# Kernel optimization log

Measured on AMD Instinct MI355X. Metric: run time of the kernel, lower is better.

## Reference

```python
import jax, jax.numpy as jnp
import numpy as np

B, V, J, NS, NE = 2048, 5023, 5, 100, 50
PB = 9 * (J - 1)  # pose basis = 36


def setup_inputs() -> dict:
    key = jax.random.key(0)
    ks = jax.random.split(key, 8)
    jr = jax.random.uniform(ks[5], (J, V), dtype=jnp.float32)
    lw = jax.random.uniform(ks[6], (V, J), dtype=jnp.float32)
    return {
        "shape_params": jax.random.normal(ks[0], (B, NS), dtype=jnp.float32),
        "expression_params": jax.random.normal(ks[1], (B, NE), dtype=jnp.float32),
        "pose": jax.random.normal(ks[2], (B, J * 3), dtype=jnp.float32) * 0.2,
        "v_template": jax.random.normal(ks[3], (V, 3), dtype=jnp.float32) * 0.1,
        "shapedirs": jax.random.normal(ks[4], (V, 3, NS + NE), dtype=jnp.float32) * 0.01,
        "posedirs": jax.random.normal(ks[7], (PB, V * 3), dtype=jnp.float32) * 0.01,
        "J_regressor": jr / jnp.sum(jr, axis=1, keepdims=True),   # rows sum to 1 (convex combos)
        "lbs_weights": lw / jnp.sum(lw, axis=1, keepdims=True),   # rows sum to 1 (skinning weights)
        "parents": np.array([0, 0, 1, 1, 1], dtype=np.int64),     # FLAME kintree (root entry unused)
    }


def batch_rodrigues(rot_vecs):
    """(N,3) axis-angle -> (N,3,3) rotation matrices (matches torch ref incl. +1e-8)."""
    angle = jnp.linalg.norm(rot_vecs + 1e-8, axis=1, keepdims=True)      # (N,1)
    rd = rot_vecs / angle
    cos = jnp.cos(angle)[:, :, None]                                      # (N,1,1)
    sin = jnp.sin(angle)[:, :, None]
    rx, ry, rz = rd[:, 0], rd[:, 1], rd[:, 2]
    z = jnp.zeros_like(rx)
    K = jnp.stack([z, -rz, ry, rz, z, -rx, -ry, rx, z], axis=1).reshape(-1, 3, 3)
    I = jnp.eye(3, dtype=rot_vecs.dtype)
    return I + sin * K + (1.0 - cos) * jnp.matmul(K, K)


def reference(shape_params, expression_params, pose, v_template, shapedirs,
              posedirs, J_regressor, lbs_weights, parents):
    par = np.asarray(parents)  # static kinematic tree
    b = shape_params.shape[0]
    betas = jnp.concatenate([shape_params, expression_params], axis=1)     # (B,150)
    v_shaped = v_template + jnp.einsum('bl,vkl->bvk', betas, shapedirs)    # (B,V,3)
    Jts = jnp.einsum('bvk,jv->bjk', v_shaped, J_regressor)                 # (B,J,3)
    # pose -> rotations, pose-corrective offsets
    rot_mats = batch_rodrigues(pose.reshape(-1, 3)).reshape(b, -1, 3, 3)   # (B,J,3,3)
    I3 = jnp.eye(3, dtype=pose.dtype)
    pose_feature = (rot_mats[:, 1:] - I3).reshape(b, -1)                   # (B,36)
    pose_offsets = jnp.matmul(pose_feature, posedirs).reshape(b, -1, 3)    # (B,V,3)
    v_posed = v_posed = pose_offsets + v_shaped
    # kinematic chain (relative joint transforms -> world transforms)
    rel_joints = jnp.concatenate(
        [Jts[:, :1], Jts[:, 1:] - Jts[:, par[1:]]], axis=1)                # (B,J,3)
    top = jnp.concatenate([rot_mats, rel_joints[..., None]], axis=-1)      # (B,J,3,4)
    bottom = jnp.broadcast_to(
        jnp.array([0., 0., 0., 1.], dtype=pose.dtype), (b, Jts.shape[1], 1, 4))
    tm = jnp.concatenate([top, bottom], axis=2)                            # (B,J,4,4)
    chain = [tm[:, 0]]
    for i in range(1, par.shape[0]):  # tiny fixed loop over 5 joints
        chain.append(jnp.matmul(chain[int(par[i])], tm[:, i]))
    transforms = jnp.stack(chain, axis=1)                                  # (B,J,4,4)
    posed_joints = transforms[:, :, :3, 3]
    # remove rest-pose joint locations: subtract (transforms @ [j;0]) from last column
    tj = jnp.einsum('bjmn,bjn->bjm', transforms[:, :, :, :3], Jts)         # (B,J,4)
    rel_transforms = transforms.at[:, :, :, 3].add(-tj)                    # (B,J,4,4)
    # linear blend skinning
    T = jnp.einsum('vj,bjmn->bvmn', lbs_weights, rel_transforms)           # (B,V,4,4)
    verts = jnp.einsum('bvmn,bvn->bvm', T[:, :, :3, :3], v_posed) + T[:, :, :3, 3]
    return verts, posed_joints
```

## Files before the change

### kernel.cpp

```cpp
#include <hip/hip_runtime.h>
#include <hip/hip_bf16.h>
#include <math.h>

#define B_N 2048
#define V_N 5023
#define V3_N 15069
#define NSJB 157
#define CHUNK 32

typedef float f32x4 __attribute__((ext_vector_type(4)));
typedef short short8 __attribute__((ext_vector_type(8)));

static __device__ __forceinline__ ushort f2bf(float f) {
  __hip_bfloat16 h = __float2bfloat16(f);
  return *reinterpret_cast<ushort*>(&h);
}

__global__ __launch_bounds__(256) void k_pre(const float* __restrict__ sdirs,
                                             const float* __restrict__ pdirs,
                                             const float* __restrict__ vtemp,
                                             const float* __restrict__ Jr,
                                             const float* __restrict__ shp,
                                             const float* __restrict__ expr,
                                             ushort* __restrict__ basis,
                                             float* __restrict__ part,
                                             ushort* __restrict__ bb) {
  __shared__ float Sh[16][452];
  __shared__ float Pd[36][48];
  int t = threadIdx.x, blk = blockIdx.x;
  if (blk < 314) {
    int bx = blk, v0 = bx * 16;
    for (int idx = t; idx < 16 * 450; idx += 256) {
      int r = idx / 450, c = idx - r * 450;
      int v = v0 + r;
      Sh[r][c] = (v < V_N) ? sdirs[(size_t)v * 450 + c] : 0.0f;
    }
    for (int idx = t; idx < 36 * 48; idx += 256) {
      int p = idx / 48, c = idx - p * 48;
      int v3 = v0 * 3 + c;
      Pd[p][c] = (v3 < V3_N) ? pdirs[(size_t)p * V3_N + v3] : 0.0f;
    }
    __syncthreads();
    for (int idx = t; idx < 64 * 96; idx += 256) {
      int row = idx / 96, kp = idx - row * 96;
      int vl = row >> 2, c = row & 3;
      int k0 = kp * 2;
      float f0 = 0.0f, f1 = 0.0f;
      if (c < 3) {
        if (k0 < 150) {
          f0 = Sh[vl][c * 150 + k0];
          f1 = Sh[vl][c * 150 + k0 + 1];
        } else if (k0 < 186) {
          f0 = Pd[k0 - 150][vl * 3 + c];
          f1 = Pd[k0 - 149][vl * 3 + c];
        }
      }
      uint u = (uint)f2bf(f0) | ((uint)f2bf(f1) << 16);
      ((uint*)basis)[(size_t)(bx * 64 + row) * 96 + kp] = u;
    }
  } else if (blk < 314 + NSJB) {
    float (*JrL)[CHUNK] = (float(*)[CHUNK]) & Sh[0][0];
    int bk = blk - 314;
    int vstart = bk * CHUNK;
    int cnt = min(CHUNK, V_N - vstart);
    for (int idx = t; idx < 5 * CHUNK; idx += 256) {
      int j = idx / CHUNK, vi = idx % CHUNK;
      JrL[j][vi] = (vi < cnt) ? Jr[j * V_N + vstart + vi] : 0.0f;
    }
    __syncthreads();
    float acc0[5] = {0, 0, 0, 0, 0}, acc1[5] = {0, 0, 0, 0, 0};
    int c0 = t, c1 = t + 256;
#pragma unroll 4
    for (int vi = 0; vi < CHUNK; ++vi) {
      int v = min(vstart + vi, V_N - 1);
      float val0 = sdirs[(size_t)v * 450 + c0];
      float val1 = 0.0f;
      if (c1 < 450) val1 = sdirs[(size_t)v * 450 + c1];
      else if (c1 < 453) val1 = vtemp[(size_t)v * 3 + (c1 - 450)];
#pragma unroll
      for (int j = 0; j < 5; ++j) {
        float w = JrL[j][vi];
        acc0[j] = fmaf(w, val0, acc0[j]);
        acc1[j] = fmaf(w, val1, acc1[j]);
      }
    }
    float* prow = part + (size_t)bk * 2280;
#pragma unroll
    for (int j = 0; j < 5; ++j) {
      prow[j * 456 + c0] = acc0[j];
      if (c1 < 453) prow[j * 456 + c1] = acc1[j];
    }
  } else {
    int idx = (blk - 314 - NSJB) * 256 + t;
    int b = idx / 96, cp = idx - b * 96;
    int c0 = cp * 2;
    float f0 = 0.0f, f1 = 0.0f;
    if (c0 < 100) {
      f0 = shp[(size_t)b * 100 + c0];
      f1 = shp[(size_t)b * 100 + c0 + 1];
    } else if (c0 < 150) {
      f0 = expr[(size_t)b * 50 + (c0 - 100)];
      f1 = expr[(size_t)b * 50 + (c0 - 99)];
    }
    ((uint*)bb)[idx] = (uint)f2bf(f0) | ((uint)f2bf(f1) << 16);
  }
}

__global__ void k_sj_reduce(const float* __restrict__ part, float* __restrict__ SJ) {
  int id = blockIdx.x * 256 + threadIdx.x;
  if (id >= 2280) return;
  int c = id % 456;
  if (c >= 453) return;
  float s = 0.0f;
  for (int bk = 0; bk < NSJB; ++bk) s += part[(size_t)bk * 2280 + id];
  SJ[id] = s;
}

__global__ __launch_bounds__(256) void k_jpose(const float* __restrict__ shp,
                                               const float* __restrict__ expr,
                                               const float* __restrict__ SJ,
                                               const float* __restrict__ pose,
                                               ushort* __restrict__ bb,
                                               float* __restrict__ A,
                                               float* __restrict__ out) {
  __shared__ float JtL[16][16];
  int t = threadIdx.x;
  int g = t >> 4, r = t & 15;
  int b = blockIdx.x * 16 + g;
  if (r < 15) {
    int j = r / 3, k = r - j * 3;
    const float* SJr = SJ + j * 456;
    float acc = SJr[450 + k];
    const float* srow = shp + (size_t)b * 100;
    const float* erow = expr + (size_t)b * 50;
    for (int l = 0; l < 100; ++l) acc = fmaf(srow[l], SJr[k * 150 + l], acc);
    for (int l = 0; l < 50; ++l) acc = fmaf(erow[l], SJr[k * 150 + 100 + l], acc);
    JtL[g][r] = acc;
  }
  __syncthreads();
  if (r != 0) return;
  float R[5][3][3];
#pragma unroll
  for (int j = 0; j < 5; ++j) {
    float rx = pose[(size_t)b * 15 + j * 3 + 0];
    float ry = pose[(size_t)b * 15 + j * 3 + 1];
    float rz = pose[(size_t)b * 15 + j * 3 + 2];
    float sx = rx + 1e-8f, sy = ry + 1e-8f, sz = rz + 1e-8f;
    float ang = sqrtf(sx * sx + sy * sy + sz * sz);
    float inv = 1.0f / ang;
    float ux = rx * inv, uy = ry * inv, uz = rz * inv;
    float c = cosf(ang), s = sinf(ang), omc = 1.0f - c;
    float K[3][3] = {{0.0f, -uz, uy}, {uz, 0.0f, -ux}, {-uy, ux, 0.0f}};
#pragma unroll
    for (int m = 0; m < 3; ++m)
#pragma unroll
      for (int n = 0; n < 3; ++n) {
        float k2 = 0.0f;
#pragma unroll
        for (int q = 0; q < 3; ++q) k2 += K[m][q] * K[q][n];
        R[j][m][n] = ((m == n) ? 1.0f : 0.0f) + s * K[m][n] + omc * k2;
      }
  }
  {
    float pf[36];
#pragma unroll
    for (int j = 1; j < 5; ++j)
#pragma unroll
      for (int m = 0; m < 3; ++m)
#pragma unroll
        for (int n = 0; n < 3; ++n)
          pf[(j - 1) * 9 + m * 3 + n] = R[j][m][n] - ((m == n) ? 1.0f : 0.0f);
    uint* bbu = (uint*)bb + (size_t)b * 96 + 75;
#pragma unroll
    for (int q = 0; q < 18; ++q)
      bbu[q] = (uint)f2bf(pf[2 * q]) | ((uint)f2bf(pf[2 * q + 1]) << 16);
  }
  float Jt[5][3];
#pragma unroll
  for (int j = 0; j < 5; ++j)
#pragma unroll
    for (int k = 0; k < 3; ++k) Jt[j][k] = JtL[g][j * 3 + k];
  const int par[5] = {0, 0, 1, 1, 1};
  float rel[5][3];
#pragma unroll
  for (int k = 0; k < 3; ++k) rel[0][k] = Jt[0][k];
#pragma unroll
  for (int j = 1; j < 5; ++j)
#pragma unroll
    for (int k = 0; k < 3; ++k) rel[j][k] = Jt[j][k] - Jt[par[j]][k];
  float Rg[5][3][3], tg[5][3];
#pragma unroll
  for (int m = 0; m < 3; ++m) {
#pragma unroll
    for (int n = 0; n < 3; ++n) Rg[0][m][n] = R[0][m][n];
    tg[0][m] = rel[0][m];
  }
#pragma unroll
  for (int j = 1; j < 5; ++j) {
    int p = par[j];
#pragma unroll
    for (int m = 0; m < 3; ++m) {
      float t2 = tg[p][m];
#pragma unroll
      for (int n = 0; n < 3; ++n) {
        float s = 0.0f;
#pragma unroll
        for (int q = 0; q < 3; ++q) s = fmaf(Rg[p][m][q], R[j][q][n], s);
        Rg[j][m][n] = s;
        t2 = fmaf(Rg[p][m][n], rel[j][n], t2);
      }
      tg[j][m] = t2;
    }
  }
#pragma unroll
  for (int j = 0; j < 5; ++j)
#pragma unroll
    for (int k = 0; k < 3; ++k)
      out[(size_t)B_N * V_N * 3 + ((size_t)b * 5 + j) * 3 + k] = tg[j][k];
  float Af[5][12];
#pragma unroll
  for (int j = 0; j < 5; ++j)
#pragma unroll
    for (int m = 0; m < 3; ++m) {
      float tj = 0.0f;
#pragma unroll
      for (int n = 0; n < 3; ++n) {
        Af[j][m * 4 + n] = Rg[j][m][n];
        tj = fmaf(Rg[j][m][n], Jt[j][n], tj);
      }
      Af[j][m * 4 + 3] = tg[j][m] - tj;
    }
  float* Ab = A + (size_t)b * 64;
#pragma unroll
  for (int q = 0; q < 12; ++q) Ab[q] = Af[0][q];
#pragma unroll
  for (int j = 1; j < 5; ++j)
#pragma unroll
    for (int q = 0; q < 12; ++q) Ab[j * 12 + q] = Af[j][q] - Af[0][q];
}

__global__ __launch_bounds__(512, 4) void k_main(const ushort* __restrict__ basis,
                                                 const ushort* __restrict__ bb,
                                                 const float* __restrict__ Amat,
                                                 const float* __restrict__ lw,
                                                 const float* __restrict__ vtemp,
                                                 float* __restrict__ out) {
  __shared__ alignas(16) ushort AL[64 * 200];
  __shared__ alignas(16) ushort BL[64 * 200];
  __shared__ alignas(16) float AmL[64 * 68];
  int t = threadIdx.x;
  int bx = blockIdx.y;
  int by = blockIdx.x;
  int b0 = by * 64;
#pragma unroll
  for (int i = 0; i < 3; ++i) {
    int c = t + i * 512;
    int r = c / 24, k = (c % 24) * 8;
    *(short8*)(&AL[r * 200 + k]) = *(const short8*)(&basis[((size_t)bx * 64 + r) * 192 + k]);
    *(short8*)(&BL[r * 200 + k]) = *(const short8*)(&bb[((size_t)(b0 + r)) * 192 + k]);
  }
#pragma unroll
  for (int i = 0; i < 2; ++i) {
    int c = t + i * 512;
    int r = c / 16, q = (c % 16) * 4;
    *(f32x4*)(&AmL[r * 68 + q]) = *(const f32x4*)(&Amat[((size_t)(b0 + r)) * 64 + q]);
  }
  __syncthreads();
  int lane = t & 63;
  int w = __builtin_amdgcn_readfirstlane(t >> 6);
  int wm = w >> 1, wn = w & 1;
  int lm = lane & 15, g = lane >> 4;
  f32x4 acc0 = {0.f, 0.f, 0.f, 0.f}, acc1 = {0.f, 0.f, 0.f, 0.f};
  const int arow = (wm * 16 + lm) * 200;
  const int brow0 = (wn * 32 + lm) * 200;
  const int brow1 = (wn * 32 + 16 + lm) * 200;
#pragma unroll
  for (int ks = 0; ks < 6; ++ks) {
    int k = ks * 32 + 8 * g;
    short8 af = *(const short8*)(&AL[arow + k]);
    short8 bf0 = *(const short8*)(&BL[brow0 + k]);
    short8 bf1 = *(const short8*)(&BL[brow1 + k]);
    acc0 = __builtin_amdgcn_mfma_f32_16x16x32_bf16(af, bf0, acc0, 0, 0, 0);
    acc1 = __builtin_amdgcn_mfma_f32_16x16x32_bf16(af, bf1, acc1, 0, 0, 0);
  }
  int v = bx * 16 + wm * 4 + g;
  bool valid = v < V_N;
  int vv = valid ? v : 0;
  float wv[4];
#pragma unroll
  for (int j = 0; j < 4; ++j) wv[j] = lw[(size_t)vv * 5 + 1 + j];
  float vt0 = vtemp[(size_t)vv * 3 + 0];
  float vt1 = vtemp[(size_t)vv * 3 + 1];
  float vt2 = vtemp[(size_t)vv * 3 + 2];
#pragma unroll
  for (int ni = 0; ni < 2; ++ni) {
    f32x4 p = ni ? acc1 : acc0;
    int bl = wn * 32 + ni * 16 + lm;
    const float* Ar = &AmL[bl * 68];
    f32x4 T0 = *(const f32x4*)(Ar + 0);
    f32x4 T1 = *(const f32x4*)(Ar + 4);
    f32x4 T2 = *(const f32x4*)(Ar + 8);
#pragma unroll
    for (int j = 1; j < 5; ++j) {
      f32x4 d0 = *(const f32x4*)(Ar + j * 12 + 0);
      f32x4 d1 = *(const f32x4*)(Ar + j * 12 + 4);
      f32x4 d2 = *(const f32x4*)(Ar + j * 12 + 8);
      float wjv = wv[j - 1];
#pragma unroll
      for (int c = 0; c < 4; ++c) {
        T0[c] = fmaf(wjv, d0[c], T0[c]);
        T1[c] = fmaf(wjv, d1[c], T1[c]);
        T2[c] = fmaf(wjv, d2[c], T2[c]);
      }
    }
    float x = p[0] + vt0, y = p[1] + vt1, z = p[2] + vt2;
    float ox = fmaf(T0[0], x, fmaf(T0[1], y, fmaf(T0[2], z, T0[3])));
    float oy = fmaf(T1[0], x, fmaf(T1[1], y, fmaf(T1[2], z, T1[3])));
    float oz = fmaf(T2[0], x, fmaf(T2[1], y, fmaf(T2[2], z, T2[3])));
    if (valid) {
      size_t o = ((size_t)(b0 + bl)) * V3_N + (size_t)v * 3;
      out[o + 0] = ox;
      out[o + 1] = oy;
      out[o + 2] = oz;
    }
  }
}

extern "C" void kernel_launch(void* const* d_in, const int* in_sizes, int n_in,
                              void* d_out, int out_size, void* d_ws, size_t ws_size,
                              hipStream_t stream) {
  const float* shp = (const float*)d_in[0];
  const float* expr = (const float*)d_in[1];
  const float* pose = (const float*)d_in[2];
  const float* vtemp = (const float*)d_in[3];
  const float* sdirs = (const float*)d_in[4];
  const float* pdirs = (const float*)d_in[5];
  const float* Jr = (const float*)d_in[6];
  const float* lw = (const float*)d_in[7];
  float* out = (float*)d_out;
  float* wsf = (float*)d_ws;

  const size_t OFF_PART = 0;
  const size_t OFF_SJ = 358400;
  const size_t OFF_A = 786688;
  const size_t OFF_BB = 917760;
  const size_t OFF_BASIS = 1114368;
  float* part = wsf + OFF_PART;
  float* SJ = wsf + OFF_SJ;
  float* A = wsf + OFF_A;
  ushort* bb = (ushort*)(wsf + OFF_BB);
  ushort* basis = (ushort*)(wsf + OFF_BASIS);

  hipLaunchKernelGGL(k_pre, dim3(314 + NSJB + 768), dim3(256), 0, stream,
                     sdirs, pdirs, vtemp, Jr, shp, expr, basis, part, bb);
  hipLaunchKernelGGL(k_sj_reduce, dim3(9), dim3(256), 0, stream, part, SJ);
  hipLaunchKernelGGL(k_jpose, dim3(128), dim3(256), 0, stream,
                     shp, expr, SJ, pose, bb, A, out);
  hipLaunchKernelGGL(k_main, dim3(32, 314), dim3(512), 0, stream,
                     basis, bb, A, lw, vtemp, out);
}
```

Measured before the change: 119.7 us.

## Swizzle k_main LDS, alias transform buffer, and fold SJ reduction into atomics

k_main drops the padded LDS layout for an XOR-swizzled one and reuses the A-tile region for the per-batch transform matrices after the MFMA loop. This cuts shared memory per block so the launch bound can rise from 4 to 6 blocks per CU, at the cost of two extra barriers. Separately, the joint-regression partial sums are now accumulated with global atomicAdd into a memset buffer, which removes the k_sj_reduce launch but adds atomic contention and makes the summation order nondeterministic.

```diff
diff --git a/kernel.cpp b/kernel.cpp
--- a/kernel.cpp
+++ b/kernel.cpp
@@ -23,7 +23,7 @@
                                              const float* __restrict__ shp,
                                              const float* __restrict__ expr,
                                              ushort* __restrict__ basis,
-                                             float* __restrict__ part,
+                                             float* __restrict__ SJ,
                                              ushort* __restrict__ bb) {
   __shared__ float Sh[16][452];
   __shared__ float Pd[36][48];
@@ -84,11 +84,10 @@
         acc1[j] = fmaf(w, val1, acc1[j]);
       }
     }
-    float* prow = part + (size_t)bk * 2280;
 #pragma unroll
     for (int j = 0; j < 5; ++j) {
-      prow[j * 456 + c0] = acc0[j];
-      if (c1 < 453) prow[j * 456 + c1] = acc1[j];
+      atomicAdd(&SJ[j * 456 + c0], acc0[j]);
+      if (c1 < 453) atomicAdd(&SJ[j * 456 + c1], acc1[j]);
     }
   } else {
     int idx = (blk - 314 - NSJB) * 256 + t;
@@ -104,16 +103,6 @@
     }
     ((uint*)bb)[idx] = (uint)f2bf(f0) | ((uint)f2bf(f1) << 16);
   }
-}
-
-__global__ void k_sj_reduce(const float* __restrict__ part, float* __restrict__ SJ) {
-  int id = blockIdx.x * 256 + threadIdx.x;
-  if (id >= 2280) return;
-  int c = id % 456;
-  if (c >= 453) return;
-  float s = 0.0f;
-  for (int bk = 0; bk < NSJB; ++bk) s += part[(size_t)bk * 2280 + id];
-  SJ[id] = s;
 }
 
 __global__ __launch_bounds__(256) void k_jpose(const float* __restrict__ shp,
@@ -239,15 +228,15 @@
     for (int q = 0; q < 12; ++q) Ab[j * 12 + q] = Af[j][q] - Af[0][q];
 }
 
-__global__ __launch_bounds__(512, 4) void k_main(const ushort* __restrict__ basis,
+__global__ __launch_bounds__(512, 6) void k_main(const ushort* __restrict__ basis,
                                                  const ushort* __restrict__ bb,
                                                  const float* __restrict__ Amat,
                                                  const float* __restrict__ lw,
                                                  const float* __restrict__ vtemp,
                                                  float* __restrict__ out) {
-  __shared__ alignas(16) ushort AL[64 * 200];
-  __shared__ alignas(16) ushort BL[64 * 200];
-  __shared__ alignas(16) float AmL[64 * 68];
+  __shared__ alignas(16) ushort AL[64 * 192];
+  __shared__ alignas(16) ushort BL[64 * 192];
+  float* AmL = (float*)AL;
   int t = threadIdx.x;
   int bx = blockIdx.y;
   int by = blockIdx.x;
@@ -255,15 +244,10 @@
 #pragma unroll
   for (int i = 0; i < 3; ++i) {
     int c = t + i * 512;
-    int r = c / 24, k = (c % 24) * 8;
-    *(short8*)(&AL[r * 200 + k]) = *(const short8*)(&basis[((size_t)bx * 64 + r) * 192 + k]);
-    *(short8*)(&BL[r * 200 + k]) = *(const short8*)(&bb[((size_t)(b0 + r)) * 192 + k]);
-  }
-#pragma unroll
-  for (int i = 0; i < 2; ++i) {
-    int c = t + i * 512;
-    int r = c / 16, q = (c % 16) * 4;
-    *(f32x4*)(&AmL[r * 68 + q]) = *(const f32x4*)(&Amat[((size_t)(b0 + r)) * 64 + q]);
+    int r = c / 24, kb = c % 24;
+    int dst = (r * 24 + (kb ^ (r & 7))) * 8;
+    *(short8*)(&AL[dst]) = *(const short8*)(&basis[((size_t)bx * 64 + r) * 192 + kb * 8]);
+    *(short8*)(&BL[dst]) = *(const short8*)(&bb[((size_t)(b0 + r)) * 192 + kb * 8]);
   }
   __syncthreads();
   int lane = t & 63;
@@ -271,15 +255,15 @@
   int wm = w >> 1, wn = w & 1;
   int lm = lane & 15, g = lane >> 4;
   f32x4 acc0 = {0.f, 0.f, 0.f, 0.f}, acc1 = {0.f, 0.f, 0.f, 0.f};
-  const int arow = (wm * 16 + lm) * 200;
-  const int brow0 = (wn * 32 + lm) * 200;
-  const int brow1 = (wn * 32 + 16 + lm) * 200;
+  const int ar = wm * 16 + lm;
+  const int br0 = wn * 32 + lm;
+  const int br1 = wn * 32 + 16 + lm;
 #pragma unroll
   for (int ks = 0; ks < 6; ++ks) {
-    int k = ks * 32 + 8 * g;
-    short8 af = *(const short8*)(&AL[arow + k]);
-    short8 bf0 = *(const short8*)(&BL[brow0 + k]);
-    short8 bf1 = *(const short8*)(&BL[brow1 + k]);
+    int kb = ks * 4 + g;
+    short8 af = *(const short8*)(&AL[(ar * 24 + (kb ^ (ar & 7))) * 8]);
+    short8 bf0 = *(const short8*)(&BL[(br0 * 24 + (kb ^ (br0 & 7))) * 8]);
+    short8 bf1 = *(const short8*)(&BL[(br1 * 24 + (kb ^ (br1 & 7))) * 8]);
     acc0 = __builtin_amdgcn_mfma_f32_16x16x32_bf16(af, bf0, acc0, 0, 0, 0);
     acc1 = __builtin_amdgcn_mfma_f32_16x16x32_bf16(af, bf1, acc1, 0, 0, 0);
   }
@@ -292,6 +276,14 @@
   float vt0 = vtemp[(size_t)vv * 3 + 0];
   float vt1 = vtemp[(size_t)vv * 3 + 1];
   float vt2 = vtemp[(size_t)vv * 3 + 2];
+  __syncthreads();
+#pragma unroll
+  for (int i = 0; i < 2; ++i) {
+    int c = t + i * 512;
+    int r = c / 16, q = (c % 16) * 4;
+    *(f32x4*)(&AmL[r * 68 + q]) = *(const f32x4*)(&Amat[((size_t)(b0 + r)) * 64 + q]);
+  }
+  __syncthreads();
 #pragma unroll
   for (int ni = 0; ni < 2; ++ni) {
     f32x4 p = ni ? acc1 : acc0;
@@ -340,20 +332,18 @@
   float* out = (float*)d_out;
   float* wsf = (float*)d_ws;
 
-  const size_t OFF_PART = 0;
   const size_t OFF_SJ = 358400;
   const size_t OFF_A = 786688;
   const size_t OFF_BB = 917760;
   const size_t OFF_BASIS = 1114368;
-  float* part = wsf + OFF_PART;
   float* SJ = wsf + OFF_SJ;
   float* A = wsf + OFF_A;
   ushort* bb = (ushort*)(wsf + OFF_BB);
   ushort* basis = (ushort*)(wsf + OFF_BASIS);
 
+  hipMemsetAsync(SJ, 0, 2280 * sizeof(float), stream);
   hipLaunchKernelGGL(k_pre, dim3(314 + NSJB + 768), dim3(256), 0, stream,
-                     sdirs, pdirs, vtemp, Jr, shp, expr, basis, part, bb);
-  hipLaunchKernelGGL(k_sj_reduce, dim3(9), dim3(256), 0, stream, part, SJ);
+                     sdirs, pdirs, vtemp, Jr, shp, expr, basis, SJ, bb);
   hipLaunchKernelGGL(k_jpose, dim3(128), dim3(256), 0, stream,
                      shp, expr, SJ, pose, bb, A, out);
   hipLaunchKernelGGL(k_main, dim3(32, 314), dim3(512), 0, stream,
```

Result: faster. 111.7 us (-6.7%).
